# Performance work log

Hardware: AMD Instinct MI355X
Metric: run time of the kernel (lower is better)

Reference implementation:

```python
import jax, jax.numpy as jnp
import numpy as np

# Module hyperparameters (from init_kwargs)
NBITS = 8
FOLD = 8
B = 8192
IN_F = 2048
OUT_F = 2048
ISIZE = IN_F // FOLD   # 256
OSIZE = OUT_F // FOLD  # 256
QMAX = 2 ** (NBITS - 1) - 1  # 127


def setup_inputs() -> dict:
    key = jax.random.key(0)
    k1, k2, k3, k4, k5 = jax.random.split(key, 5)
    inp = jax.random.normal(k1, (B, IN_F), dtype=jnp.float32)
    # per-fold linear weights, torch nn.Linear default-ish scale
    W = jax.random.normal(k2, (FOLD, OSIZE, ISIZE), dtype=jnp.float32) * (1.0 / np.sqrt(ISIZE))
    # UniformPositionalEncoding buffers: offset + per-fold per-column ranges
    pe = jax.random.normal(k3, (1, FOLD, ISIZE), dtype=jnp.float32) * 0.1
    min_range = -jax.random.uniform(k4, (1, FOLD, ISIZE), minval=0.25, maxval=1.0, dtype=jnp.float32)
    max_range = jax.random.uniform(k5, (1, FOLD, ISIZE), minval=0.25, maxval=1.0, dtype=jnp.float32)
    return {"input": inp, "W": W, "pe": pe, "min_range": min_range, "max_range": max_range}


def reference(input, W, pe, min_range, max_range):
    b = input.shape[0]
    x = input.reshape(b, FOLD, ISIZE)
    # QuantAct symmetric, clamp_only=True: per-tensor scale s = max|x| / n, clamp to [-s*n, s*n]
    s = jnp.max(jnp.abs(x)) / QMAX
    x = jnp.clip(x, -s * QMAX, s * QMAX)
    s = s * QMAX  # scaled range multiplier
    # positional offset, broadcast over batch
    x = x + pe[0]  # [b, FOLD, ISIZE]
    x_flat = x.reshape(b * FOLD, ISIZE)

    def per_fold(Wi, mn, mx):
        # fold_idx_ste forward passes full x through; range mask zeroes out-of-range entries
        mask = (x_flat < mn * s) | (x_flat > mx * s)  # [b*FOLD, ISIZE]
        xm = jnp.where(mask, jnp.float32(0.0), x_flat)
        o = xm @ Wi.T  # [b*FOLD, OSIZE]
        return o.reshape(b, FOLD, OSIZE).sum(axis=1)  # [b, OSIZE]

    # vmap over the FOLD small linears
    out = jax.vmap(per_fold)(W, min_range[0], max_range[0])  # [FOLD, b, OSIZE]
    out = jnp.transpose(out, (1, 0, 2)).reshape(b, FOLD * OSIZE)  # stack dim=1 then flatten
    return out
```

## Files before the change

### kernel.cpp

```cpp
#include <hip/hip_runtime.h>

#define FOLD  8
#define ISIZE 256
#define IN_F  2048
#define OUT_F 2048
#define TBM   32
#define NBLK  (8192 / TBM)
#define CHW   1104

typedef __attribute__((ext_vector_type(8))) short short8;
typedef __attribute__((ext_vector_type(4))) float f32x4;

__device__ __forceinline__ unsigned f2bf(float f) {
    unsigned u = __float_as_uint(f);
    u += 0x7FFFu + ((u >> 16) & 1u);
    return (u >> 16);
}

__global__ __launch_bounds__(256)
void absmax_kernel(const float4* __restrict__ in,
                   float* __restrict__ partials,
                   unsigned int* __restrict__ scal, int mode) {
    const int idx = blockIdx.x * 256 + threadIdx.x;
    float m0 = 0.f, m1 = 0.f, m2 = 0.f, m3 = 0.f;
    #pragma unroll
    for (int k = 0; k < 64; k += 4) {
        float4 a = in[idx + (k    ) * 65536];
        float4 b = in[idx + (k + 1) * 65536];
        float4 c = in[idx + (k + 2) * 65536];
        float4 d = in[idx + (k + 3) * 65536];
        m0 = fmaxf(m0, fmaxf(fmaxf(fabsf(a.x), fabsf(a.y)), fmaxf(fabsf(a.z), fabsf(a.w))));
        m1 = fmaxf(m1, fmaxf(fmaxf(fabsf(b.x), fabsf(b.y)), fmaxf(fabsf(b.z), fabsf(b.w))));
        m2 = fmaxf(m2, fmaxf(fmaxf(fabsf(c.x), fabsf(c.y)), fmaxf(fabsf(c.z), fabsf(c.w))));
        m3 = fmaxf(m3, fmaxf(fmaxf(fabsf(d.x), fabsf(d.y)), fmaxf(fabsf(d.z), fabsf(d.w))));
    }
    float m = fmaxf(fmaxf(m0, m1), fmaxf(m2, m3));
    #pragma unroll
    for (int off = 32; off > 0; off >>= 1)
        m = fmaxf(m, __shfl_down(m, off, 64));
    __shared__ float sm[4];
    int lane = threadIdx.x & 63, wv = threadIdx.x >> 6;
    if (lane == 0) sm[wv] = m;
    __syncthreads();
    if (threadIdx.x == 0) {
        float r = fmaxf(fmaxf(sm[0], sm[1]), fmaxf(sm[2], sm[3]));
        if (mode) partials[blockIdx.x] = r;
        else      atomicMax(scal, __float_as_uint(r));
    }
}

__global__ void convert_w_kernel(const float* __restrict__ W,
                                 unsigned short* __restrict__ wsw) {
    int t    = blockIdx.x * 256 + threadIdx.x;
    int wid  = t >> 6;
    int lane = t & 63;
    int i  = wid >> 7;
    int nt = (wid >> 3) & 15;
    int ks = wid & 7;
    int n = lane & 15, q = lane >> 4;
    const float* src = W + (((size_t)i * 256 + nt * 16 + n) * 256 + ks * 32 + q * 8);
    float4 s0 = *(const float4*)(src);
    float4 s1 = *(const float4*)(src + 4);
    uint4 p;
    p.x = f2bf(s0.x) | (f2bf(s0.y) << 16);
    p.y = f2bf(s0.z) | (f2bf(s0.w) << 16);
    p.z = f2bf(s1.x) | (f2bf(s1.y) << 16);
    p.w = f2bf(s1.z) | (f2bf(s1.w) << 16);
    *(uint4*)(wsw + (size_t)wid * 512 + lane * 8) = p;
}

template<int PRECONV>
__global__ __launch_bounds__(512, 2)
void fold_main(const float* __restrict__ in,
               const float* __restrict__ W,
               const unsigned short* __restrict__ wsw,
               const float* __restrict__ pe,
               const float* __restrict__ mn,
               const float* __restrict__ mx,
               const float* __restrict__ partials,
               const unsigned int* __restrict__ scal,
               int npart,
               float* __restrict__ out) {
    __shared__ __align__(16) unsigned short ylds[64 * CHW];
    __shared__ float sred[8];

    const int tid  = threadIdx.x;
    const int lane = tid & 63;
    const int wv   = tid >> 6;
    const int row0 = blockIdx.x * TBM;

    float mabs;
    if (npart > 0) {
        float v = (tid < npart) ? partials[tid] : 0.0f;
        #pragma unroll
        for (int off = 32; off > 0; off >>= 1)
            v = fmaxf(v, __shfl_down(v, off, 64));
        if (lane == 0) sred[wv] = v;
        __syncthreads();
        float r = sred[0];
        #pragma unroll
        for (int i = 1; i < 8; ++i) r = fmaxf(r, sred[i]);
        mabs = r;
    } else {
        mabs = __uint_as_float(*scal);
    }
    const float c = (mabs / 127.0f) * 127.0f;

    {
        const int kp  = tid & 127;
        const int rq  = tid >> 7;
        const int k0  = kp * 2;
        const int jh  = kp & 3;
        const int qA  = (kp >> 2) & 3;
        const int ksA = kp >> 4;

        float pef[FOLD][2], lo[FOLD][2], hi[FOLD][2];
        #pragma unroll
        for (int f = 0; f < FOLD; ++f) {
            float2 p2 = *(const float2*)(pe + f * ISIZE + k0);
            pef[f][0] = p2.x; pef[f][1] = p2.y;
        }
        #pragma unroll
        for (int i = 0; i < FOLD; ++i) {
            float2 a2 = *(const float2*)(mn + i * ISIZE + k0);
            float2 b2 = *(const float2*)(mx + i * ISIZE + k0);
            lo[i][0] = a2.x * c; lo[i][1] = a2.y * c;
            hi[i][0] = b2.x * c; hi[i][1] = b2.y * c;
        }

        #pragma unroll
        for (int r8 = 0; r8 < 8; ++r8) {
            const int row = rq * 8 + r8;
            const float* rowp = in + (size_t)(row0 + row) * IN_F + k0;
            float2 xr[FOLD];
            #pragma unroll
            for (int f = 0; f < FOLD; ++f) xr[f] = *(const float2*)(rowp + f * ISIZE);

            float acc[FOLD][2];
            #pragma unroll
            for (int i = 0; i < FOLD; ++i) { acc[i][0] = 0.0f; acc[i][1] = 0.0f; }
            #pragma unroll
            for (int f = 0; f < FOLD; ++f) {
                float xv0 = fminf(fmaxf(xr[f].x, -c), c) + pef[f][0];
                float xv1 = fminf(fmaxf(xr[f].y, -c), c) + pef[f][1];
                #pragma unroll
                for (int i = 0; i < FOLD; ++i) {
                    if (xv0 >= lo[i][0] && xv0 <= hi[i][0]) acc[i][0] += xv0;
                    if (xv1 >= lo[i][1] && xv1 <= hi[i][1]) acc[i][1] += xv1;
                }
            }
            const unsigned base = (unsigned)((row >> 4) * 544 + qA * 136 + (row & 15) * 8 + jh * 2);
            #pragma unroll
            for (int i = 0; i < FOLD; ++i) {
                unsigned us = f2bf(acc[i][0]) | (f2bf(acc[i][1]) << 16);
                *(unsigned*)&ylds[(i * 8 + ksA) * CHW + base] = us;
            }
        }
    }
    __syncthreads();

    {
        const int fi   = wv;
        const int mrow = lane & 15;
        const int quad = lane >> 4;

        short8 afr[8][2];
        #pragma unroll
        for (int kk = 0; kk < 8; ++kk) {
            #pragma unroll
            for (int mt = 0; mt < 2; ++mt)
                afr[kk][mt] = *(const short8*)&ylds[(fi * 8 + kk) * CHW + mt * 544 + quad * 136 + mrow * 8];
        }

        const int col0 = fi * 256 + mrow;
        #pragma unroll 2
        for (int nt = 0; nt < 16; ++nt) {
            f32x4 a0 = (f32x4){0.f, 0.f, 0.f, 0.f};
            f32x4 a1 = (f32x4){0.f, 0.f, 0.f, 0.f};
            if (PRECONV) {
                const unsigned short* wb = wsw + ((size_t)(fi * 16 + nt) * 8) * 512 + lane * 8;
                uint4 wq[8];
                #pragma unroll
                for (int kk = 0; kk < 8; ++kk) wq[kk] = *(const uint4*)(wb + kk * 512);
                #pragma unroll
                for (int kk = 0; kk < 8; ++kk) {
                    union { uint4 u; short8 s; } cv; cv.u = wq[kk];
                    a0 = __builtin_amdgcn_mfma_f32_16x16x32_bf16(afr[kk][0], cv.s, a0, 0, 0, 0);
                    a1 = __builtin_amdgcn_mfma_f32_16x16x32_bf16(afr[kk][1], cv.s, a1, 0, 0, 0);
                }
            } else {
                const float* wb = W + ((size_t)(fi * 256 + nt * 16 + mrow) * 256 + quad * 8);
                float4 w[16];
                #pragma unroll
                for (int kk = 0; kk < 8; ++kk) {
                    w[2 * kk]     = *(const float4*)(wb + kk * 32);
                    w[2 * kk + 1] = *(const float4*)(wb + kk * 32 + 4);
                }
                #pragma unroll
                for (int kk = 0; kk < 8; ++kk) {
                    union { uint4 u; short8 s; } cv;
                    cv.u.x = f2bf(w[2*kk].x)   | (f2bf(w[2*kk].y)   << 16);
                    cv.u.y = f2bf(w[2*kk].z)   | (f2bf(w[2*kk].w)   << 16);
                    cv.u.z = f2bf(w[2*kk+1].x) | (f2bf(w[2*kk+1].y) << 16);
                    cv.u.w = f2bf(w[2*kk+1].z) | (f2bf(w[2*kk+1].w) << 16);
                    a0 = __builtin_amdgcn_mfma_f32_16x16x32_bf16(afr[kk][0], cv.s, a0, 0, 0, 0);
                    a1 = __builtin_amdgcn_mfma_f32_16x16x32_bf16(afr[kk][1], cv.s, a1, 0, 0, 0);
                }
            }
            #pragma unroll
            for (int rg = 0; rg < 4; ++rg) {
                out[(size_t)(row0 +      quad * 4 + rg) * OUT_F + col0 + nt * 16] = a0[rg];
                out[(size_t)(row0 + 16 + quad * 4 + rg) * OUT_F + col0 + nt * 16] = a1[rg];
            }
        }
    }
}

extern "C" void kernel_launch(void* const* d_in, const int* in_sizes, int n_in,
                              void* d_out, int out_size, void* d_ws, size_t ws_size,
                              hipStream_t stream) {
    const float* in = (const float*)d_in[0];
    const float* W  = (const float*)d_in[1];
    const float* pe = (const float*)d_in[2];
    const float* mn = (const float*)d_in[3];
    const float* mx = (const float*)d_in[4];
    float* out = (float*)d_out;

    const size_t PART_OFF  = 16;
    const size_t WSW_OFF   = 4096;
    const size_t WSW_BYTES = (size_t)FOLD * 256 * 256 * 2;

    unsigned int*   scal     = (unsigned int*)d_ws;
    float*          partials = (float*)((char*)d_ws + PART_OFF);
    unsigned short* wsw      = (unsigned short*)((char*)d_ws + WSW_OFF);

    const bool twostage = ws_size >= PART_OFF + 256 * sizeof(float);
    const bool preconv  = ws_size >= WSW_OFF + WSW_BYTES;

    if (!twostage) hipMemsetAsync(d_ws, 0, sizeof(unsigned int), stream);

    absmax_kernel<<<256, 256, 0, stream>>>((const float4*)in, partials, scal,
                                           twostage ? 1 : 0);
    const int npart = twostage ? 256 : 0;
    if (preconv) {
        convert_w_kernel<<<256, 256, 0, stream>>>(W, wsw);
        fold_main<1><<<NBLK, 512, 0, stream>>>(in, W, wsw, pe, mn, mx,
                                               partials, scal, npart, out);
    } else {
        fold_main<0><<<NBLK, 512, 0, stream>>>(in, W, wsw, pe, mn, mx,
                                               partials, scal, npart, out);
    }
}
```

Before: 153.6 us.

## Use 1024-thread blocks in fold_main and widen absmax grid

The main fused kernel now launches 1024 threads per block instead of 512. Each thread handles 4 rows instead of 8 in the masked-sum stage, and each pair of waves splits a fold's 16 N-tiles in half in the MFMA stage. The absmax pre-pass gets a configurable per-thread quota and runs on 1024 blocks with 16 loads each, producing 1024 partials that the main kernel reduces. The aim is more parallelism per block and a shorter serial chain per thread. The cost is more partials to reduce per block, and the weight fragments loaded for a fold are now shared across two waves. With launch bounds of (1024,1), the ~141KB LDS per block still allows one block per CU.

```diff
diff --git a/kernel.cpp b/kernel.cpp
--- a/kernel.cpp
+++ b/kernel.cpp
@@ -20,21 +20,17 @@
 __global__ __launch_bounds__(256)
 void absmax_kernel(const float4* __restrict__ in,
                    float* __restrict__ partials,
-                   unsigned int* __restrict__ scal, int mode) {
+                   unsigned int* __restrict__ scal,
+                   int quota, int mode) {
+    const int nthreads = gridDim.x * 256;
     const int idx = blockIdx.x * 256 + threadIdx.x;
-    float m0 = 0.f, m1 = 0.f, m2 = 0.f, m3 = 0.f;
-    #pragma unroll
-    for (int k = 0; k < 64; k += 4) {
-        float4 a = in[idx + (k    ) * 65536];
-        float4 b = in[idx + (k + 1) * 65536];
-        float4 c = in[idx + (k + 2) * 65536];
-        float4 d = in[idx + (k + 3) * 65536];
-        m0 = fmaxf(m0, fmaxf(fmaxf(fabsf(a.x), fabsf(a.y)), fmaxf(fabsf(a.z), fabsf(a.w))));
-        m1 = fmaxf(m1, fmaxf(fmaxf(fabsf(b.x), fabsf(b.y)), fmaxf(fabsf(b.z), fabsf(b.w))));
-        m2 = fmaxf(m2, fmaxf(fmaxf(fabsf(c.x), fabsf(c.y)), fmaxf(fabsf(c.z), fabsf(c.w))));
-        m3 = fmaxf(m3, fmaxf(fmaxf(fabsf(d.x), fabsf(d.y)), fmaxf(fabsf(d.z), fabsf(d.w))));
-    }
-    float m = fmaxf(fmaxf(m0, m1), fmaxf(m2, m3));
+    float m = 0.f;
+    #pragma unroll 4
+    for (int q = 0; q < quota; ++q) {
+        float4 a = in[idx + q * nthreads];
+        m = fmaxf(m, fmaxf(fmaxf(fabsf(a.x), fabsf(a.y)),
+                           fmaxf(fabsf(a.z), fabsf(a.w))));
+    }
     #pragma unroll
     for (int off = 32; off > 0; off >>= 1)
         m = fmaxf(m, __shfl_down(m, off, 64));
@@ -70,7 +66,7 @@
 }
 
 template<int PRECONV>
-__global__ __launch_bounds__(512, 2)
+__global__ __launch_bounds__(1024, 1)
 void fold_main(const float* __restrict__ in,
                const float* __restrict__ W,
                const unsigned short* __restrict__ wsw,
@@ -82,7 +78,7 @@
                int npart,
                float* __restrict__ out) {
     __shared__ __align__(16) unsigned short ylds[64 * CHW];
-    __shared__ float sred[8];
+    __shared__ float sred[16];
 
     const int tid  = threadIdx.x;
     const int lane = tid & 63;
@@ -99,7 +95,7 @@
         __syncthreads();
         float r = sred[0];
         #pragma unroll
-        for (int i = 1; i < 8; ++i) r = fmaxf(r, sred[i]);
+        for (int i = 1; i < 16; ++i) r = fmaxf(r, sred[i]);
         mabs = r;
     } else {
         mabs = __uint_as_float(*scal);
@@ -129,8 +125,8 @@
         }
 
         #pragma unroll
-        for (int r8 = 0; r8 < 8; ++r8) {
-            const int row = rq * 8 + r8;
+        for (int r4 = 0; r4 < 4; ++r4) {
+            const int row = rq * 4 + r4;
             const float* rowp = in + (size_t)(row0 + row) * IN_F + k0;
             float2 xr[FOLD];
             #pragma unroll
@@ -160,7 +156,8 @@
     __syncthreads();
 
     {
-        const int fi   = wv;
+        const int fi   = wv >> 1;
+        const int nh   = wv & 1;
         const int mrow = lane & 15;
         const int quad = lane >> 4;
 
@@ -174,11 +171,12 @@
 
         const int col0 = fi * 256 + mrow;
         #pragma unroll 2
-        for (int nt = 0; nt < 16; ++nt) {
+        for (int nt8 = 0; nt8 < 8; ++nt8) {
+            const int ntg = nh * 8 + nt8;
             f32x4 a0 = (f32x4){0.f, 0.f, 0.f, 0.f};
             f32x4 a1 = (f32x4){0.f, 0.f, 0.f, 0.f};
             if (PRECONV) {
-                const unsigned short* wb = wsw + ((size_t)(fi * 16 + nt) * 8) * 512 + lane * 8;
+                const unsigned short* wb = wsw + ((size_t)(fi * 16 + ntg) * 8) * 512 + lane * 8;
                 uint4 wq[8];
                 #pragma unroll
                 for (int kk = 0; kk < 8; ++kk) wq[kk] = *(const uint4*)(wb + kk * 512);
@@ -189,7 +187,7 @@
                     a1 = __builtin_amdgcn_mfma_f32_16x16x32_bf16(afr[kk][1], cv.s, a1, 0, 0, 0);
                 }
             } else {
-                const float* wb = W + ((size_t)(fi * 256 + nt * 16 + mrow) * 256 + quad * 8);
+                const float* wb = W + ((size_t)(fi * 256 + ntg * 16 + mrow) * 256 + quad * 8);
                 float4 w[16];
                 #pragma unroll
                 for (int kk = 0; kk < 8; ++kk) {
@@ -209,8 +207,8 @@
             }
             #pragma unroll
             for (int rg = 0; rg < 4; ++rg) {
-                out[(size_t)(row0 +      quad * 4 + rg) * OUT_F + col0 + nt * 16] = a0[rg];
-                out[(size_t)(row0 + 16 + quad * 4 + rg) * OUT_F + col0 + nt * 16] = a1[rg];
+                out[(size_t)(row0 +      quad * 4 + rg) * OUT_F + col0 + ntg * 16] = a0[rg];
+                out[(size_t)(row0 + 16 + quad * 4 + rg) * OUT_F + col0 + ntg * 16] = a1[rg];
             }
         }
     }
@@ -227,27 +225,34 @@
     float* out = (float*)d_out;
 
     const size_t PART_OFF  = 16;
-    const size_t WSW_OFF   = 4096;
+    const size_t WSW_OFF   = 8192;
     const size_t WSW_BYTES = (size_t)FOLD * 256 * 256 * 2;
 
     unsigned int*   scal     = (unsigned int*)d_ws;
     float*          partials = (float*)((char*)d_ws + PART_OFF);
     unsigned short* wsw      = (unsigned short*)((char*)d_ws + WSW_OFF);
 
-    const bool twostage = ws_size >= PART_OFF + 256 * sizeof(float);
-    const bool preconv  = ws_size >= WSW_OFF + WSW_BYTES;
-
-    if (!twostage) hipMemsetAsync(d_ws, 0, sizeof(unsigned int), stream);
-
-    absmax_kernel<<<256, 256, 0, stream>>>((const float4*)in, partials, scal,
-                                           twostage ? 1 : 0);
-    const int npart = twostage ? 256 : 0;
+    const bool preconv = ws_size >= WSW_OFF + WSW_BYTES;
+
+    int npart;
+    if (ws_size >= PART_OFF + 1024 * sizeof(float)) {
+        absmax_kernel<<<1024, 256, 0, stream>>>((const float4*)in, partials, scal, 16, 1);
+        npart = 1024;
+    } else if (ws_size >= PART_OFF + 256 * sizeof(float)) {
+        absmax_kernel<<<256, 256, 0, stream>>>((const float4*)in, partials, scal, 64, 1);
+        npart = 256;
+    } else {
+        hipMemsetAsync(d_ws, 0, sizeof(unsigned int), stream);
+        absmax_kernel<<<256, 256, 0, stream>>>((const float4*)in, partials, scal, 64, 0);
+        npart = 0;
+    }
+
     if (preconv) {
         convert_w_kernel<<<256, 256, 0, stream>>>(W, wsw);
-        fold_main<1><<<NBLK, 512, 0, stream>>>(in, W, wsw, pe, mn, mx,
-                                               partials, scal, npart, out);
+        fold_main<1><<<NBLK, 1024, 0, stream>>>(in, W, wsw, pe, mn, mx,
+                                                partials, scal, npart, out);
     } else {
-        fold_main<0><<<NBLK, 512, 0, stream>>>(in, W, wsw, pe, mn, mx,
-                                               partials, scal, npart, out);
-    }
-}
+        fold_main<0><<<NBLK, 1024, 0, stream>>>(in, W, wsw, pe, mn, mx,
+                                                partials, scal, npart, out);
+    }
+}
```

Result: no change. 152.8 us (-0.5%).
